# Optimization experiments

Hardware: AMD Instinct MI355X
Metric: run time of the kernel (lower is better)

The kernel has to match this reference:

```python
import jax, jax.numpy as jnp
import numpy as np

B, S, H = 1, 2048, 2048
NH, NKV, HD = 32, 8, 64
RBS, ICS, RBN = 64, 64, 16          # retrieval_block_size, input_chunk_size, retrieval_block_num
RLEN = RBS * RBN                     # 1024 retrieval tokens
KV = RLEN + S                        # 3072 total kv length
START = RLEN                         # INPUT_START_IDX
SCALE = HD ** -0.5
NEG = -1e9


def _document_ids():
    # mirrors get_document_ids
    ids = np.full(KV, -1, np.int32)
    ids[:START] = np.arange(START) // RBS + 1            # retrieval blocks -> 1..RBN
    chunk = np.arange(S) // ICS
    ids[START:] = np.where(chunk == 0, -1, np.minimum(chunk, RBN))
    return ids


def _block_mask():
    # mirrors causal_retrieval_mask_mod, precomputed dense [S, KV]
    ids = _document_ids()
    qpos = np.arange(S) + START
    kv = np.arange(KV)
    causal = (qpos[:, None] >= kv[None, :]) & (kv[None, :] > START)
    doc = (ids[qpos][:, None] == ids[None, :]) & (kv[None, :] < START)
    return jnp.asarray(causal | doc)


_MASK = _block_mask()


def _rotate_half(x):
    h = x.shape[-1] // 2
    return jnp.concatenate([-x[..., h:], x[..., :h]], axis=-1)


def setup_inputs() -> dict:
    key = jax.random.key(0)
    ks = jax.random.split(key, 6)
    inv_freq = 1.0 / (10000.0 ** (np.arange(0, HD, 2, dtype=np.float32) / HD))
    ang = np.arange(S, dtype=np.float32)[:, None] * inv_freq[None, :]   # [S, HD/2]
    emb = np.concatenate([ang, ang], axis=-1)                            # [S, HD]
    cos = jnp.asarray(np.cos(emb))[None].astype(jnp.float32)            # [1, S, HD]
    sin = jnp.asarray(np.sin(emb))[None].astype(jnp.float32)
    return {
        "hidden_states": jax.random.normal(ks[0], (B, S, H), jnp.float32),
        "cos": cos,
        "sin": sin,
        "retrieval_key": jax.random.normal(ks[1], (B, NKV, RLEN, HD), jnp.float32),
        "retrieval_value": jax.random.normal(ks[2], (B, NKV, RLEN, HD), jnp.float32),
        "Wq": jax.random.normal(ks[3], (H, NH * HD), jnp.float32) * 0.02,
        "Wk": jax.random.normal(ks[4], (H, NKV * HD), jnp.float32) * 0.02,
        "Wv": jax.random.normal(ks[5], (H, NKV * HD), jnp.float32) * 0.02,
        "Wo": jax.random.normal(jax.random.fold_in(key, 7), (NH * HD, H), jnp.float32) * 0.02,
    }


def reference(hidden_states, cos, sin, retrieval_key, retrieval_value, Wq, Wk, Wv, Wo):
    # QKV projections -> [B, nheads, S, HD]
    q = (hidden_states @ Wq).reshape(B, S, NH, HD).transpose(0, 2, 1, 3)
    k = (hidden_states @ Wk).reshape(B, S, NKV, HD).transpose(0, 2, 1, 3)
    v = (hidden_states @ Wv).reshape(B, S, NKV, HD).transpose(0, 2, 1, 3)
    # RoPE (retrieval kv is pre-encoded; rope only on current tokens)
    c, s = cos[:, None, :, :], sin[:, None, :, :]
    q = q * c + _rotate_half(q) * s
    k = k * c + _rotate_half(k) * s
    # prepend retrieval kv
    k = jnp.concatenate([retrieval_key, k], axis=2)    # [B, NKV, KV, HD]
    v = jnp.concatenate([retrieval_value, v], axis=2)
    # GQA: expand kv heads
    g = NH // NKV
    k = jnp.repeat(k, g, axis=1)                        # [B, NH, KV, HD]
    v = jnp.repeat(v, g, axis=1)
    scores = jnp.einsum("bhqd,bhkd->bhqk", q, k) * SCALE
    scores = jnp.where(_MASK[None, None], scores, NEG)
    probs = jax.nn.softmax(scores, axis=-1)
    # fully-masked rows (q_idx 0) -> zero output, matching flex_attention
    row_valid = _MASK.any(axis=-1)[None, None, :, None]
    probs = jnp.where(row_valid, probs, 0.0)
    out = jnp.einsum("bhqk,bhkd->bhqd", probs, v)
    out = out.transpose(0, 2, 1, 3).reshape(B, S, NH * HD)
    return out @ Wo
```

## Files before the change

### kernel.cpp

```cpp
#include <hip/hip_runtime.h>

#define S_LEN 2048
#define H_DIM 2048
#define NH 32
#define NKV 8
#define HD 64
#define RLEN 1024
#define KVTOT 3072
#define SCALE 0.125f
#define QS 0.18033688011112042f
#define FIX8 11.541560327111707f

typedef unsigned short ushort_t;
using short8 = __attribute__((ext_vector_type(8))) short;
using f32x4 = __attribute__((ext_vector_type(4))) float;

__device__ __forceinline__ float b2f(unsigned short u) {
    union { unsigned int i; float f; } v;
    v.i = ((unsigned int)u) << 16;
    return v.f;
}
__device__ __forceinline__ unsigned short f2b(float f) {
    union { float f; unsigned int i; } v;
    v.f = f;
    unsigned int x = v.i;
    return (unsigned short)((x + 0x7fffu + ((x >> 16) & 1u)) >> 16);
}

__device__ __forceinline__ void gload16(const ushort_t* g, ushort_t* l) {
    __builtin_amdgcn_global_load_lds(
        (const __attribute__((address_space(1))) unsigned int*)g,
        (__attribute__((address_space(3))) unsigned int*)l, 16, 0, 0);
}

__device__ __forceinline__ int is_f32(const void* p) {
    const unsigned int* w = (const unsigned int*)p;
    const int lane = threadIdx.x & 63;
    int cnt = 0;
#pragma unroll
    for (int j = 0; j < 4; ++j) {
        unsigned int lo = w[lane + j * 64] & 0xFFFFu;
        unsigned int e = (lo >> 7) & 0xFFu;
        cnt += (lo != 0u && (e < 90u || e > 140u)) ? 1 : 0;
    }
    unsigned long long b = __ballot(cnt >= 2);
    return __popcll(b) > 16;
}

__device__ __forceinline__ int qswz(int row, int cb) { return cb ^ (row & 31); }

__global__ __launch_bounds__(256) void prep_all(
    const void* __restrict__ rk, const void* __restrict__ rv,
    const void* __restrict__ Wq, const void* __restrict__ Wk,
    const void* __restrict__ Wv, const void* __restrict__ Wo,
    ushort_t* __restrict__ WqkvT, ushort_t* __restrict__ WoT,
    ushort_t* __restrict__ ktall, ushort_t* __restrict__ vtall,
    const void* __restrict__ hs, ushort_t* __restrict__ hsb)
{
    __shared__ ushort_t S[64 * 72];
    const int id = blockIdx.x;
    if (id >= 2944) {
        const int F = is_f32(hs);
        int i = ((id - 2944) * 256 + threadIdx.x) * 8;
        ushort_t o[8];
        if (F) {
            const float* p = (const float*)hs + i;
            float4 f0 = ((const float4*)p)[0];
            float4 f1 = ((const float4*)p)[1];
            o[0] = f2b(f0.x); o[1] = f2b(f0.y); o[2] = f2b(f0.z); o[3] = f2b(f0.w);
            o[4] = f2b(f1.x); o[5] = f2b(f1.y); o[6] = f2b(f1.z); o[7] = f2b(f1.w);
            *(uint4*)(hsb + i) = *(const uint4*)o;
        } else {
            *(uint4*)(hsb + i) = *(const uint4*)((const ushort_t*)hs + i);
        }
        return;
    }
    if (id < 2560) {
        int z, t;
        if (id < 1024)      { z = 0; t = id; }
        else if (id < 1280) { z = 1; t = id - 1024; }
        else if (id < 1536) { z = 2; t = id - 1280; }
        else                { z = 3; t = id - 1536; }
        const void* src = (z == 0) ? Wq : (z == 1) ? Wk : (z == 2) ? Wv : Wo;
        const int F = is_f32(src);
        const int C = (z == 1 || z == 2) ? 512 : 2048;
        const int nx = (z == 1 || z == 2) ? 8 : 32;
        const int x = t % nx, y = t / nx;
        ushort_t* dst = (z == 3) ? WoT : WqkvT;
        const int rofs = (z == 1) ? 2048 : (z == 2) ? 2560 : 0;

        const int r0 = y * 64, c0 = x * 64;
        const int lr = threadIdx.x >> 2, lc = (threadIdx.x & 3) * 16;
        ushort_t tt[16];
        if (F) {
            const float* p = (const float*)src + (size_t)(r0 + lr) * C + c0 + lc;
#pragma unroll
            for (int j = 0; j < 16; j += 4) {
                float4 f = *(const float4*)(p + j);
                tt[j] = f2b(f.x); tt[j + 1] = f2b(f.y); tt[j + 2] = f2b(f.z); tt[j + 3] = f2b(f.w);
            }
        } else {
            const ushort_t* p = (const ushort_t*)src + (size_t)(r0 + lr) * C + c0 + lc;
            *(uint4*)tt = ((const uint4*)p)[0];
            *(uint4*)(tt + 8) = ((const uint4*)p)[1];
        }
        *(uint4*)&S[lr * 72 + lc] = *(const uint4*)tt;
        *(uint4*)&S[lr * 72 + lc + 8] = *(const uint4*)(tt + 8);
        __syncthreads();
        const int wc = threadIdx.x >> 2, wr = (threadIdx.x & 3) * 16;
        ushort_t o[16];
#pragma unroll
        for (int j = 0; j < 16; ++j) o[j] = S[(wr + j) * 72 + wc];
        ushort_t* q = dst + (size_t)(rofs + c0 + wc) * 2048 + r0 + wr;
        *(uint4*)q = *(const uint4*)o;
        *(uint4*)(q + 8) = *(const uint4*)(o + 8);
    } else if (id < 2816) {
        const int kF = is_f32(rk);
        const int e = ((id - 2560) * 256 + threadIdx.x) * 8;
        const int kvh = e >> 16;
        const int rem = e & 65535;
        ushort_t* dst = ktall + (size_t)kvh * (KVTOT * 64) + rem;
        if (kF) {
            const float* p = (const float*)rk + e;
            float4 f0 = ((const float4*)p)[0];
            float4 f1 = ((const float4*)p)[1];
            ushort_t o[8];
            o[0] = f2b(f0.x); o[1] = f2b(f0.y); o[2] = f2b(f0.z); o[3] = f2b(f0.w);
            o[4] = f2b(f1.x); o[5] = f2b(f1.y); o[6] = f2b(f1.z); o[7] = f2b(f1.w);
            *(uint4*)dst = *(const uint4*)o;
        } else {
            *(uint4*)dst = *(const uint4*)((const ushort_t*)rk + e);
        }
    } else {
        const int idv = id - 2816;
        const int t = idv & 15;
        const int kvh = idv >> 4;
        const int vF = is_f32(rv);
        const int lr = threadIdx.x >> 2, lc = (threadIdx.x & 3) * 16;
        ushort_t tt[16];
        size_t base = ((size_t)kvh * RLEN + t * 64 + lr) * HD + lc;
        if (vF) {
            const float* p = (const float*)rv + base;
#pragma unroll
            for (int j = 0; j < 16; j += 4) {
                float4 f = *(const float4*)(p + j);
                tt[j] = f2b(f.x); tt[j + 1] = f2b(f.y); tt[j + 2] = f2b(f.z); tt[j + 3] = f2b(f.w);
            }
        } else {
            const ushort_t* p = (const ushort_t*)rv + base;
            *(uint4*)tt = ((const uint4*)p)[0];
            *(uint4*)(tt + 8) = ((const uint4*)p)[1];
        }
        *(uint4*)&S[lr * 72 + lc] = *(const uint4*)tt;
        *(uint4*)&S[lr * 72 + lc + 8] = *(const uint4*)(tt + 8);
        __syncthreads();
        const int wc = threadIdx.x >> 2, wr = (threadIdx.x & 3) * 16;
        ushort_t o[16];
#pragma unroll
        for (int j = 0; j < 16; ++j) o[j] = S[(wr + j) * 72 + wc];
        const int blk = t * 2 + (wr >> 5);
        ushort_t* q = vtall + (((size_t)(kvh * 96 + blk) * 64 + wc) * 32) + (wr & 31);
        *(uint4*)q = *(const uint4*)o;
        *(uint4*)(q + 8) = *(const uint4*)(o + 8);
    }
}

__global__ __launch_bounds__(256, 4) void gemm_qkv(
    const ushort_t* __restrict__ A, const ushort_t* __restrict__ Bt,
    ushort_t* __restrict__ qkvp, ushort_t* __restrict__ ktall,
    ushort_t* __restrict__ vtall,
    const void* __restrict__ cosv, const void* __restrict__ sinv)
{
    const int K = 2048;
    __shared__ __align__(16) ushort_t As[2][64 * 32];
    __shared__ __align__(16) ushort_t Bs[2][128 * 32];
    const int tid = threadIdx.x;
    const int wave = tid >> 6, lane = tid & 63;
    const int lq = lane & 15, quad = lane >> 4;
    const int m0 = blockIdx.y * 64, n0 = blockIdx.x * 128;
    const int wm = (wave & 1) * 32, wn = (wave >> 1) * 64;
    const int nk = K >> 5;

    const int srow = wave * 16 + (lane >> 2);
    const int scol = ((lane & 3) ^ ((lane >> 3) & 3)) * 8;
    const ushort_t* ga  = A  + (size_t)(m0 + srow) * K + scol;
    const ushort_t* gb0 = Bt + (size_t)(n0 + srow) * K + scol;
    const ushort_t* gb1 = Bt + (size_t)(n0 + 64 + srow) * K + scol;
    ushort_t* lA = &As[0][0] + wave * 16 * 32;
    ushort_t* lB = &Bs[0][0] + wave * 16 * 32;
    const int rs = (lq >> 1) & 3;

    f32x4 acc[2][4];
#pragma unroll
    for (int i = 0; i < 2; ++i)
#pragma unroll
        for (int j = 0; j < 4; ++j) acc[i][j] = (f32x4){0.f, 0.f, 0.f, 0.f};

#define STAGE_G(buf, kt) do { \
        gload16(ga  + (size_t)(kt) * 32, lA + (buf) * (64 * 32)); \
        gload16(gb0 + (size_t)(kt) * 32, lB + (buf) * (128 * 32)); \
        gload16(gb1 + (size_t)(kt) * 32, lB + (buf) * (128 * 32) + 64 * 32); \
    } while (0)

    STAGE_G(0, 0);
    int cur = 0;
    for (int kt = 0; kt < nk; ++kt) {
        if (kt + 1 < nk) {
            STAGE_G(cur ^ 1, kt + 1);
            asm volatile("s_waitcnt vmcnt(3)" ::: "memory");
        } else {
            asm volatile("s_waitcnt vmcnt(0)" ::: "memory");
        }
        __builtin_amdgcn_s_barrier();
        __builtin_amdgcn_sched_barrier(0);
        short8 afr[2], bfr[4];
#pragma unroll
        for (int i = 0; i < 2; ++i)
            afr[i] = *(const short8*)&As[cur][(wm + i * 16 + lq) * 32 + (quad ^ rs) * 8];
#pragma unroll
        for (int j = 0; j < 4; ++j)
            bfr[j] = *(const short8*)&Bs[cur][(wn + j * 16 + lq) * 32 + (quad ^ rs) * 8];
#pragma unroll
        for (int i = 0; i < 2; ++i)
#pragma unroll
            for (int j = 0; j < 4; ++j)
                acc[i][j] = __builtin_amdgcn_mfma_f32_16x16x32_bf16(afr[i], bfr[j], acc[i][j], 0, 0, 0);
        __builtin_amdgcn_s_barrier();
        cur ^= 1;
    }
#undef STAGE_G

    if (n0 < 2048) {
        const int cb = (n0 + wn) >> 6;
#pragma unroll
        for (int i = 0; i < 2; ++i)
#pragma unroll
            for (int r = 0; r < 4; ++r) {
                const int si = m0 + wm + i * 16 + quad * 4 + r;
                ushort_t* cp = qkvp + (size_t)si * 2048 + (qswz(si, cb) << 6) + lq;
#pragma unroll
                for (int j = 0; j < 4; ++j) cp[j * 16] = f2b(acc[i][j][r]);
            }
    } else if (n0 < 2560) {
        const int cF = is_f32(cosv), sF = is_f32(sinv);
        const int kvh = (n0 - 2048 + wn) >> 6;
#pragma unroll
        for (int i = 0; i < 2; ++i)
#pragma unroll
            for (int r = 0; r < 4; ++r) {
                const int si = m0 + wm + i * 16 + quad * 4 + r;
                const int ci = si * HD + lq;
                float c0, c1, c2, c3, s0, s1, s2, s3;
                if (cF) {
                    const float* cp = (const float*)cosv + ci;
                    c0 = cp[0]; c1 = cp[16]; c2 = cp[32]; c3 = cp[48];
                } else {
                    const ushort_t* cp = (const ushort_t*)cosv + ci;
                    c0 = b2f(cp[0]); c1 = b2f(cp[16]); c2 = b2f(cp[32]); c3 = b2f(cp[48]);
                }
                if (sF) {
                    const float* sp = (const float*)sinv + ci;
                    s0 = sp[0]; s1 = sp[16]; s2 = sp[32]; s3 = sp[48];
                } else {
                    const ushort_t* sp = (const ushort_t*)sinv + ci;
                    s0 = b2f(sp[0]); s1 = b2f(sp[16]); s2 = b2f(sp[32]); s3 = b2f(sp[48]);
                }
                ushort_t* kp = ktall + ((size_t)kvh * KVTOT + RLEN + si) * HD + lq;
                kp[0]  = f2b(acc[i][0][r] * c0 - acc[i][2][r] * s0);
                kp[16] = f2b(acc[i][1][r] * c1 - acc[i][3][r] * s1);
                kp[32] = f2b(acc[i][2][r] * c2 + acc[i][0][r] * s2);
                kp[48] = f2b(acc[i][3][r] * c3 + acc[i][1][r] * s3);
            }
    } else {
        const int kvh = (n0 - 2560 + wn) >> 6;
#pragma unroll
        for (int i = 0; i < 2; ++i) {
            const int si0 = m0 + wm + i * 16 + quad * 4;
            const int blk = 32 + (si0 >> 5);
            const int slot = si0 & 31;
#pragma unroll
            for (int j = 0; j < 4; ++j) {
                const int d = j * 16 + lq;
                ushort_t o[4];
#pragma unroll
                for (int r = 0; r < 4; ++r) o[r] = f2b(acc[i][j][r]);
                *(uint2*)(vtall + ((size_t)(kvh * 96 + blk) * 64 + d) * 32 + slot) = *(const uint2*)o;
            }
        }
    }
}

__global__ __launch_bounds__(256, 4) void gemm_fin(
    const ushort_t* __restrict__ A, const ushort_t* __restrict__ Bt,
    void* __restrict__ Cv, int N, int K, const void* __restrict__ hs)
{
    const int oF = is_f32(hs);
    __shared__ __align__(16) ushort_t As[2][64 * 32];
    __shared__ __align__(16) ushort_t Bs[2][128 * 32];
    const int tid = threadIdx.x;
    const int wave = tid >> 6, lane = tid & 63;
    const int lq = lane & 15, quad = lane >> 4;
    const int m0 = blockIdx.y * 64, n0 = blockIdx.x * 128;
    const int wm = (wave & 1) * 32, wn = (wave >> 1) * 64;
    const int nk = K >> 5;

    const int srow = wave * 16 + (lane >> 2);
    const int scol = ((lane & 3) ^ ((lane >> 3) & 3)) * 8;
    const ushort_t* ga  = A  + (size_t)(m0 + srow) * K + scol;
    const ushort_t* gb0 = Bt + (size_t)(n0 + srow) * K + scol;
    const ushort_t* gb1 = Bt + (size_t)(n0 + 64 + srow) * K + scol;
    ushort_t* lA = &As[0][0] + wave * 16 * 32;
    ushort_t* lB = &Bs[0][0] + wave * 16 * 32;
    const int rs = (lq >> 1) & 3;

    f32x4 acc[2][4];
#pragma unroll
    for (int i = 0; i < 2; ++i)
#pragma unroll
        for (int j = 0; j < 4; ++j) acc[i][j] = (f32x4){0.f, 0.f, 0.f, 0.f};

#define STAGE_G(buf, kt) do { \
        gload16(ga  + (size_t)(kt) * 32, lA + (buf) * (64 * 32)); \
        gload16(gb0 + (size_t)(kt) * 32, lB + (buf) * (128 * 32)); \
        gload16(gb1 + (size_t)(kt) * 32, lB + (buf) * (128 * 32) + 64 * 32); \
    } while (0)

    STAGE_G(0, 0);
    int cur = 0;
    for (int kt = 0; kt < nk; ++kt) {
        if (kt + 1 < nk) {
            STAGE_G(cur ^ 1, kt + 1);
            asm volatile("s_waitcnt vmcnt(3)" ::: "memory");
        } else {
            asm volatile("s_waitcnt vmcnt(0)" ::: "memory");
        }
        __builtin_amdgcn_s_barrier();
        __builtin_amdgcn_sched_barrier(0);
        short8 afr[2], bfr[4];
#pragma unroll
        for (int i = 0; i < 2; ++i)
            afr[i] = *(const short8*)&As[cur][(wm + i * 16 + lq) * 32 + (quad ^ rs) * 8];
#pragma unroll
        for (int j = 0; j < 4; ++j)
            bfr[j] = *(const short8*)&Bs[cur][(wn + j * 16 + lq) * 32 + (quad ^ rs) * 8];
#pragma unroll
        for (int i = 0; i < 2; ++i)
#pragma unroll
            for (int j = 0; j < 4; ++j)
                acc[i][j] = __builtin_amdgcn_mfma_f32_16x16x32_bf16(afr[i], bfr[j], acc[i][j], 0, 0, 0);
        __builtin_amdgcn_s_barrier();
        cur ^= 1;
    }

#pragma unroll
    for (int i = 0; i < 2; ++i)
#pragma unroll
        for (int r = 0; r < 4; ++r) {
            size_t off = (size_t)(m0 + wm + i * 16 + quad * 4 + r) * N + n0 + wn + lq;
            if (oF) {
                float* cp = (float*)Cv + off;
#pragma unroll
                for (int j = 0; j < 4; ++j) cp[j * 16] = acc[i][j][r];
            } else {
                ushort_t* cp = (ushort_t*)Cv + off;
#pragma unroll
                for (int j = 0; j < 4; ++j) cp[j * 16] = f2b(acc[i][j][r]);
            }
        }
#undef STAGE_G
}

__global__ __launch_bounds__(256) void fattn(
    const ushort_t* __restrict__ qkvp, const ushort_t* __restrict__ ktall,
    const ushort_t* __restrict__ vtall, ushort_t* __restrict__ attno,
    const void* __restrict__ cosv, const void* __restrict__ sinv)
{
    const int cF = is_f32(cosv), sF = is_f32(sinv);
    const int h = blockIdx.x;
    const int yy = blockIdx.y;
    const int st = yy >> 3, r8 = yy & 7;
    const int qb = (st == 0) ? (31 - r8) : (st == 1) ? (16 + r8)
                 : (st == 2) ? (15 - r8) : r8;
    const int kvh = h >> 2;
    const int tid = threadIdx.x;
    const int wave = tid >> 6;
    const int lane = tid & 63;
    const int lq = lane & 15;
    const int quad = lane >> 4;
    const int rb64 = ((qb < 17 ? qb : 16) - 1) * 64;
    const int qrow = qb * 64 + wave * 16 + lq;

    __shared__ __align__(16) ushort_t Ks[128 * 72];
    __shared__ __align__(16) ushort_t Ps[4 * 16 * 136];
    ushort_t* pw = &Ps[wave * 16 * 136];

    short8 qfrag[2];
    {
        const int row_g = qb * 64 + wave * 16 + lq;
        const ushort_t* qrp = qkvp + (size_t)row_g * 2048 + (qswz(row_g, h) << 6);
        short8 t0 = *(const short8*)(qrp + quad * 8);
        short8 t1 = *(const short8*)(qrp + 32 + quad * 8);
        const int ci = row_g * HD + quad * 8;
        float c0[8], c1[8], s0[8], s1[8];
        if (cF) {
            const float* cp = (const float*)cosv + ci;
#pragma unroll
            for (int j = 0; j < 8; ++j) { c0[j] = cp[j]; c1[j] = cp[j + 32]; }
        } else {
            const ushort_t* cp = (const ushort_t*)cosv + ci;
#pragma unroll
            for (int j = 0; j < 8; ++j) { c0[j] = b2f(cp[j]); c1[j] = b2f(cp[j + 32]); }
        }
        if (sF) {
            const float* sp = (const float*)sinv + ci;
#pragma unroll
            for (int j = 0; j < 8; ++j) { s0[j] = sp[j]; s1[j] = sp[j + 32]; }
        } else {
            const ushort_t* sp = (const ushort_t*)sinv + ci;
#pragma unroll
            for (int j = 0; j < 8; ++j) { s0[j] = b2f(sp[j]); s1[j] = b2f(sp[j + 32]); }
        }
#pragma unroll
        for (int j = 0; j < 8; ++j) {
            float a = b2f((unsigned short)t0[j]), b = b2f((unsigned short)t1[j]);
            qfrag[0][j] = (short)f2b((a * c0[j] - b * s0[j]) * QS);
            qfrag[1][j] = (short)f2b((b * c1[j] + a * s1[j]) * QS);
        }
    }

    f32x4 oacc[4];
#pragma unroll
    for (int nt = 0; nt < 4; ++nt) oacc[nt] = (f32x4){0.f, 0.f, 0.f, 0.f};
    float lsum = 0.f;

    const int Lq = (qb > 0) ? qb * 64 + 128 : 64;
    const int nch = (Lq + 127) >> 7;
    const ushort_t* kbase = ktall + (size_t)kvh * KVTOT * HD;
    const ushort_t* vbase = vtall + (size_t)kvh * 96 * 2048;

    for (int c = 0; c < nch; ++c) {
        uint4 kreg0, kreg1, kreg2, kreg3;
        const int krow = tid >> 1;
        const int kd0 = (tid & 1) * 32;
        {
            int p = c * 128 + krow;
            uint4 z = {0, 0, 0, 0};
            kreg0 = z; kreg1 = z; kreg2 = z; kreg3 = z;
            if (p < Lq) {
                int pk = (qb > 0) ? ((p < 64) ? rb64 + p : 960 + p) : RLEN + p;
                const uint4* s = (const uint4*)(kbase + (size_t)pk * HD + kd0);
                kreg0 = s[0]; kreg1 = s[1]; kreg2 = s[2]; kreg3 = s[3];
            }
        }
        int vblk[4];
#pragma unroll
        for (int kc = 0; kc < 4; ++kc) {
            int p = c * 128 + kc * 32;
            int pk = (qb > 0) ? ((p < 64) ? rb64 + p : 960 + p) : RLEN + p;
            if (pk > KVTOT - 1) pk = KVTOT - 1;
            vblk[kc] = pk >> 5;
        }
        short8 vfA[4], vfB[4];
#pragma unroll
        for (int ntd = 0; ntd < 4; ++ntd)
            vfA[ntd] = *(const short8*)(vbase + ((size_t)vblk[0] * 64 + ntd * 16 + lq) * 32 + quad * 8);
#pragma unroll
        for (int ntd = 0; ntd < 4; ++ntd)
            vfB[ntd] = *(const short8*)(vbase + ((size_t)vblk[1] * 64 + ntd * 16 + lq) * 32 + quad * 8);

        {
            uint4* dk = (uint4*)&Ks[krow * 72 + kd0];
            dk[0] = kreg0; dk[1] = kreg1; dk[2] = kreg2; dk[3] = kreg3;
        }
        __syncthreads();

        const bool lastc = (c == nch - 1) || (qb == 0);
#pragma unroll
        for (int nt = 0; nt < 8; ++nt) {
            f32x4 a = (f32x4){-FIX8, -FIX8, -FIX8, -FIX8};
            a = __builtin_amdgcn_mfma_f32_16x16x32_bf16(
                *(const short8*)&Ks[(nt * 16 + lq) * 72 + quad * 8], qfrag[0], a, 0, 0, 0);
            a = __builtin_amdgcn_mfma_f32_16x16x32_bf16(
                *(const short8*)&Ks[(nt * 16 + lq) * 72 + 32 + quad * 8], qfrag[1], a, 0, 0, 0);
            float pex[4];
#pragma unroll
            for (int rr = 0; rr < 4; ++rr) {
                const int p = c * 128 + nt * 16 + quad * 4 + rr;
                float pexp = exp2f(a[rr]);
                if (lastc) {
                    bool valid;
                    if (qb > 0) valid = (p < 64) || ((p - 64) >= 1 && (p - 64) <= qrow);
                    else        valid = (p >= 1 && p <= qrow);
                    if (!valid) pexp = 0.f;
                } else if (c == 0) {
                    if (p == 64) pexp = 0.f;
                }
                lsum += pexp;
                pex[rr] = pexp;
            }
            unsigned int w0, w1;
            asm("v_cvt_pk_bf16_f32 %0, %1, %2" : "=v"(w0) : "v"(pex[0]), "v"(pex[1]));
            asm("v_cvt_pk_bf16_f32 %0, %1, %2" : "=v"(w1) : "v"(pex[2]), "v"(pex[3]));
            *(uint2*)&pw[lq * 136 + nt * 16 + quad * 4] = make_uint2(w0, w1);
        }

#pragma unroll
        for (int kc = 0; kc < 4; ++kc) {
            short8 pa = *(const short8*)&pw[lq * 136 + kc * 32 + quad * 8];
            short8 vf0, vf1, vf2, vf3;
            if (kc == 0)      { vf0 = vfA[0]; vf1 = vfA[1]; vf2 = vfA[2]; vf3 = vfA[3]; }
            else if (kc == 1) { vf0 = vfB[0]; vf1 = vfB[1]; vf2 = vfB[2]; vf3 = vfB[3]; }
            else {
                const int b = vblk[kc];
                vf0 = *(const short8*)(vbase + ((size_t)b * 64 + 0 * 16 + lq) * 32 + quad * 8);
                vf1 = *(const short8*)(vbase + ((size_t)b * 64 + 1 * 16 + lq) * 32 + quad * 8);
                vf2 = *(const short8*)(vbase + ((size_t)b * 64 + 2 * 16 + lq) * 32 + quad * 8);
                vf3 = *(const short8*)(vbase + ((size_t)b * 64 + 3 * 16 + lq) * 32 + quad * 8);
            }
            oacc[0] = __builtin_amdgcn_mfma_f32_16x16x32_bf16(pa, vf0, oacc[0], 0, 0, 0);
            oacc[1] = __builtin_amdgcn_mfma_f32_16x16x32_bf16(pa, vf1, oacc[1], 0, 0, 0);
            oacc[2] = __builtin_amdgcn_mfma_f32_16x16x32_bf16(pa, vf2, oacc[2], 0, 0, 0);
            oacc[3] = __builtin_amdgcn_mfma_f32_16x16x32_bf16(pa, vf3, oacc[3], 0, 0, 0);
        }
        __syncthreads();
    }

    float tot = lsum;
    tot += __shfl_xor(tot, 16, 64);
    tot += __shfl_xor(tot, 32, 64);
#pragma unroll
    for (int rr = 0; rr < 4; ++rr) {
        const int qg = qb * 64 + wave * 16 + quad * 4 + rr;
        const float tr = __shfl(tot, quad * 4 + rr, 64);
        const float inv = (qg == 0) ? 0.f : 1.f / tr;
        ushort_t* orow = attno + (size_t)qg * 2048 + h * HD;
#pragma unroll
        for (int nt = 0; nt < 4; ++nt)
            orow[nt * 16 + lq] = f2b(oacc[nt][rr] * inv);
    }
}

extern "C" void kernel_launch(void* const* d_in, const int* in_sizes, int n_in,
                              void* d_out, int out_size, void* d_ws, size_t ws_size,
                              hipStream_t stream) {
    const void* hs   = d_in[0];
    const void* cosv = d_in[1];
    const void* sinv = d_in[2];
    const void* rk   = d_in[3];
    const void* rv   = d_in[4];
    const void* Wq   = d_in[5];
    const void* Wk   = d_in[6];
    const void* Wv   = d_in[7];
    const void* Wo   = d_in[8];

    char* ws = (char*)d_ws;
    ushort_t* ktall = (ushort_t*)ws;
    ushort_t* vtall = (ushort_t*)(ws + (3u  << 20));
    ushort_t* WqkvT = (ushort_t*)(ws + (6u  << 20));
    ushort_t* WoT   = (ushort_t*)(ws + (18u << 20));
    ushort_t* qkvp  = (ushort_t*)(ws + (26u << 20));
    ushort_t* attno = WqkvT;
    ushort_t* hsb   = (ushort_t*)d_out;

    prep_all<<<4992, 256, 0, stream>>>(rk, rv, Wq, Wk, Wv, Wo, WqkvT, WoT, ktall, vtall, hs, hsb);

    gemm_qkv<<<dim3(24, 32), 256, 0, stream>>>(hsb, WqkvT, qkvp, ktall, vtall, cosv, sinv);

    fattn<<<dim3(NH, 32), 256, 0, stream>>>(qkvp, ktall, vtall, attno, cosv, sinv);

    gemm_fin<<<dim3(16, 32), 256, 0, stream>>>(attno, WoT, d_out, 2048, 2048, hs);
}
```

Measured before the change: 251.9 us.

## Split KV range of long query blocks across two workgroups with atomic merge

Query blocks 16 and above now have their KV chunk loop split in half, each half handled by a separate workgroup. A lookup table sets the launch order of the 48 y-blocks to balance load across CUs. Partial unnormalized outputs and row sums are accumulated in fp32 buffers using atomics, which need a preceding memset. A new merge kernel then normalizes and converts the result to bf16. This targets tail imbalance from causal attention, at the cost of an extra memset, an extra kernel, and fp32 atomic traffic.

```diff
diff --git a/kernel.cpp b/kernel.cpp
--- a/kernel.cpp
+++ b/kernel.cpp
@@ -48,6 +48,15 @@
 }
 
 __device__ __forceinline__ int qswz(int row, int cb) { return cb ^ (row & 31); }
+
+__device__ const signed char QB_TBL[48] = {
+    31,15,30,29,27,13,24,23,  31,30,29,28,14,25,11,12,
+    28,27,26,26,25,21,20,19,  24,23,22,22,21,19, 9,10,
+    20,16, 8, 6, 5,18,17,16,   0, 1, 2, 4, 3,18,17, 7};
+__device__ const signed char HF_TBL[48] = {
+    1,0,0,0,1,0,1,1,  0,1,1,1,0,0,0,0,
+    0,0,1,0,1,0,1,1,  0,0,1,0,1,0,0,0,
+    0,0,0,0,0,1,1,1,  0,0,0,0,0,0,0,0};
 
 __global__ __launch_bounds__(256) void prep_all(
     const void* __restrict__ rk, const void* __restrict__ rv,
@@ -372,15 +381,15 @@
 
 __global__ __launch_bounds__(256) void fattn(
     const ushort_t* __restrict__ qkvp, const ushort_t* __restrict__ ktall,
-    const ushort_t* __restrict__ vtall, ushort_t* __restrict__ attno,
+    const ushort_t* __restrict__ vtall, float* __restrict__ attacc,
+    float* __restrict__ lsacc,
     const void* __restrict__ cosv, const void* __restrict__ sinv)
 {
     const int cF = is_f32(cosv), sF = is_f32(sinv);
     const int h = blockIdx.x;
     const int yy = blockIdx.y;
-    const int st = yy >> 3, r8 = yy & 7;
-    const int qb = (st == 0) ? (31 - r8) : (st == 1) ? (16 + r8)
-                 : (st == 2) ? (15 - r8) : r8;
+    const int qb = QB_TBL[yy];
+    const int hf = HF_TBL[yy];
     const int kvh = h >> 2;
     const int tid = threadIdx.x;
     const int wave = tid >> 6;
@@ -435,10 +444,12 @@
 
     const int Lq = (qb > 0) ? qb * 64 + 128 : 64;
     const int nch = (Lq + 127) >> 7;
+    int cBeg = 0, cEnd = nch;
+    if (qb >= 16) { const int mid = nch >> 1; if (hf) cBeg = mid; else cEnd = mid; }
     const ushort_t* kbase = ktall + (size_t)kvh * KVTOT * HD;
     const ushort_t* vbase = vtall + (size_t)kvh * 96 * 2048;
 
-    for (int c = 0; c < nch; ++c) {
+    for (int c = cBeg; c < cEnd; ++c) {
         uint4 kreg0, kreg1, kreg2, kreg3;
         const int krow = tid >> 1;
         const int kd0 = (tid & 1) * 32;
@@ -528,16 +539,42 @@
     float tot = lsum;
     tot += __shfl_xor(tot, 16, 64);
     tot += __shfl_xor(tot, 32, 64);
+    const bool solo = (qb < 16);
 #pragma unroll
     for (int rr = 0; rr < 4; ++rr) {
         const int qg = qb * 64 + wave * 16 + quad * 4 + rr;
-        const float tr = __shfl(tot, quad * 4 + rr, 64);
-        const float inv = (qg == 0) ? 0.f : 1.f / tr;
-        ushort_t* orow = attno + (size_t)qg * 2048 + h * HD;
-#pragma unroll
-        for (int nt = 0; nt < 4; ++nt)
-            orow[nt * 16 + lq] = f2b(oacc[nt][rr] * inv);
-    }
+        float* orow = attacc + (size_t)qg * 2048 + h * HD;
+        if (solo) {
+#pragma unroll
+            for (int nt = 0; nt < 4; ++nt) orow[nt * 16 + lq] = oacc[nt][rr];
+        } else {
+#pragma unroll
+            for (int nt = 0; nt < 4; ++nt) atomicAdd(&orow[nt * 16 + lq], oacc[nt][rr]);
+        }
+    }
+    if (quad == 0) {
+        const int row = qb * 64 + wave * 16 + lq;
+        if (solo) lsacc[row * 32 + h] = tot;
+        else      atomicAdd(&lsacc[row * 32 + h], tot);
+    }
+}
+
+__global__ __launch_bounds__(256) void merge_o(
+    const float* __restrict__ attacc, const float* __restrict__ lsacc,
+    ushort_t* __restrict__ attno)
+{
+    const int row = blockIdx.x;
+    const int c0 = threadIdx.x * 8;
+    const float* a = attacc + (size_t)row * 2048 + c0;
+    float inv = 0.f;
+    if (row > 0) {
+        const float ls = lsacc[row * 32 + (c0 >> 6)];
+        inv = (ls > 0.f) ? 1.f / ls : 0.f;
+    }
+    ushort_t o[8];
+#pragma unroll
+    for (int j = 0; j < 8; ++j) o[j] = f2b(a[j] * inv);
+    *(uint4*)(attno + (size_t)row * 2048 + c0) = *(const uint4*)o;
 }
 
 extern "C" void kernel_launch(void* const* d_in, const int* in_sizes, int n_in,
@@ -556,17 +593,23 @@
     char* ws = (char*)d_ws;
     ushort_t* ktall = (ushort_t*)ws;
     ushort_t* vtall = (ushort_t*)(ws + (3u  << 20));
-    ushort_t* WqkvT = (ushort_t*)(ws + (6u  << 20));
-    ushort_t* WoT   = (ushort_t*)(ws + (18u << 20));
-    ushort_t* qkvp  = (ushort_t*)(ws + (26u << 20));
-    ushort_t* attno = WqkvT;
+    ushort_t* qkvp  = (ushort_t*)(ws + (6u  << 20));
+    ushort_t* WoT   = (ushort_t*)(ws + (14u << 20));
+    ushort_t* WqkvT = (ushort_t*)(ws + (22u << 20));
+    float*    attacc= (float*)(ws + (22u << 20));
+    float*    lsacc = (float*)(ws + (38u << 20));
+    ushort_t* attno = qkvp;
     ushort_t* hsb   = (ushort_t*)d_out;
 
     prep_all<<<4992, 256, 0, stream>>>(rk, rv, Wq, Wk, Wv, Wo, WqkvT, WoT, ktall, vtall, hs, hsb);
 
     gemm_qkv<<<dim3(24, 32), 256, 0, stream>>>(hsb, WqkvT, qkvp, ktall, vtall, cosv, sinv);
 
-    fattn<<<dim3(NH, 32), 256, 0, stream>>>(qkvp, ktall, vtall, attno, cosv, sinv);
+    hipMemsetAsync(ws + (22u << 20), 0, (16u << 20) + 2048 * 32 * 4, stream);
+
+    fattn<<<dim3(NH, 48), 256, 0, stream>>>(qkvp, ktall, vtall, attacc, lsacc, cosv, sinv);
+
+    merge_o<<<2048, 256, 0, stream>>>(attacc, lsacc, attno);
 
     gemm_fin<<<dim3(16, 32), 256, 0, stream>>>(attno, WoT, d_out, 2048, 2048, hs);
 }
```

Result: slower. 268.0 us (+6.4%).
